# Optimization experiments

Measured on AMD Instinct MI355X. Metric: run time of the kernel, lower is better.

Reference implementation:

```python
import jax, jax.numpy as jnp
import numpy as np

B, L, H, E, V, X = 128, 1024, 256, 128, 50000, 100


def setup_inputs() -> dict:
    key = jax.random.key(0)
    ks = jax.random.split(key, 24)
    s = 0.02
    n = lambda k, shp: jax.random.normal(k, shp, dtype=jnp.float32) * s
    inp = {
        "y_t": jax.random.randint(ks[0], (B,), 0, V),
        "h0": n(ks[1], (B, H)),
        "c0": n(ks[2], (B, H)),
        "enc_outs": jax.random.normal(ks[3], (B, L, 2 * H), dtype=jnp.float32),
        "enc_feats": jax.random.normal(ks[4], (B * L, 2 * H), dtype=jnp.float32),
        "enc_padding_mask": jnp.ones((B, L), dtype=jnp.float32),
        "c_t_1": n(ks[5], (B, 2 * H)),
        "extra_zeros": jnp.zeros((B, X), dtype=jnp.float32),
        "enc_batch_extend_vocab": jax.random.randint(ks[6], (B, L), 0, V + X),
        "coverage": jnp.zeros((B, L), dtype=jnp.float32),
        # learned parameters (torch Linear convention: y = x @ W.T + b)
        "embed_W": n(ks[7], (V, E)),
        "Wih": n(ks[8], (4 * H, E)),
        "Whh": n(ks[9], (4 * H, H)),
        "bih": jnp.zeros((4 * H,), jnp.float32),
        "bhh": jnp.zeros((4 * H,), jnp.float32),
        "xctx_W": n(ks[10], (E, 2 * H + E)),
        "xctx_b": jnp.zeros((E,), jnp.float32),
        "Ws_W": n(ks[11], (2 * H, 2 * H)),
        "Ws_b": jnp.zeros((2 * H,), jnp.float32),
        "Wc_W": n(ks[12], (2 * H, 1)),
        "v_W": n(ks[13], (1, 2 * H)),
        "pgen_W": n(ks[14], (1, 4 * H + E)),
        "pgen_b": jnp.zeros((1,), jnp.float32),
        "proj_W": n(ks[15], (H, 3 * H)),
        "proj_b": jnp.zeros((H,), jnp.float32),
        "out_W": n(ks[16], (V, H)),
        "out_b": jnp.zeros((V,), jnp.float32),
    }
    return inp


def reference(y_t, h0, c0, enc_outs, enc_feats, enc_padding_mask, c_t_1,
              extra_zeros, enc_batch_extend_vocab, coverage,
              embed_W, Wih, Whh, bih, bhh, xctx_W, xctx_b, Ws_W, Ws_b,
              Wc_W, v_W, pgen_W, pgen_b, proj_W, proj_b, out_W, out_b):
    b, l = coverage.shape
    hd = h0.shape[1]
    # embedding + input-feeding context projection
    emb = embed_W[y_t]                                        # [B,E]
    x = jnp.concatenate([c_t_1, emb], axis=1) @ xctx_W.T + xctx_b  # [B,E]
    # single LSTM step (torch gate order i,f,g,o)
    gates = x @ Wih.T + bih + h0 @ Whh.T + bhh                # [B,4H]
    i_g, f_g, g_g, o_g = jnp.split(gates, 4, axis=1)
    c = jax.nn.sigmoid(f_g) * c0 + jax.nn.sigmoid(i_g) * jnp.tanh(g_g)
    h = jax.nn.sigmoid(o_g) * jnp.tanh(c)
    s_t_hat = jnp.concatenate([h, c], axis=1)                 # [B,2H]
    # coverage attention
    dec_feats = s_t_hat @ Ws_W.T + Ws_b                       # [B,2H]
    cov_feats = coverage.reshape(-1, 1) @ Wc_W.T              # [B*L,2H]
    feats = (enc_feats.reshape(b, l, 2 * hd)
             + dec_feats[:, None, :]
             + cov_feats.reshape(b, l, 2 * hd))
    energy = jnp.tanh(feats) @ v_W[0]                         # [B,L]
    a = jax.nn.softmax(energy, axis=1) * enc_padding_mask
    a = a / jnp.sum(a, axis=1, keepdims=True)
    c_t = jnp.einsum('bl,bld->bd', a, enc_outs)               # [B,2H]
    coverage_next = coverage + a
    # generation probability
    p_gen = jax.nn.sigmoid(
        jnp.concatenate([c_t, s_t_hat, x], axis=1) @ pgen_W.T + pgen_b)  # [B,1]
    # vocab distribution
    out_hid = jnp.concatenate([h, c_t], axis=1) @ proj_W.T + proj_b      # [B,H]
    logits = out_hid @ out_W.T + out_b                                    # [B,V]
    vocab_dist = p_gen * jax.nn.softmax(logits, axis=1)
    attn_dist_ = (1.0 - p_gen) * a
    # extended vocab + pointer scatter-add
    vd_ext = jnp.concatenate([vocab_dist, extra_zeros], axis=1)          # [B,V+X]
    rows = jnp.arange(b)[:, None]
    final_dist = vd_ext.at[rows, enc_batch_extend_vocab].add(attn_dist_)
    return (final_dist, h, c, c_t, a, p_gen, coverage_next)
```

## Files before the change

kernel.cpp:

```cpp
#include <hip/hip_runtime.h>
#include <hip/hip_bf16.h>
#include <cstdint>
#include <cstddef>

#define B_   128
#define L_   1024
#define H_   256
#define E_   128
#define V_   50000
#define X_   100
#define VX_  50100
#define LSTR 50112

#define OUT_H    6412800
#define OUT_C    6445568
#define OUT_CT   6478336
#define OUT_A    6543872
#define OUT_PGEN 6674944
#define OUT_COV  6675072

typedef __attribute__((ext_vector_type(8))) short bf16x8;
typedef __attribute__((ext_vector_type(4))) float f32x4;
typedef __attribute__((ext_vector_type(8))) unsigned short u16x8;

__device__ inline float bf2f(unsigned short u){
  union { unsigned int i; float f; } v; v.i = ((unsigned int)u) << 16; return v.f;
}
__device__ inline unsigned short f2bf(float f){
  union { float f; unsigned int i; } v; v.f = f;
  unsigned int lsb = (v.i >> 16) & 1u;
  v.i += 0x7fffu + lsb;
  return (unsigned short)(v.i >> 16);
}
__device__ inline float sigm(float x){ return __builtin_amdgcn_rcpf(1.f + __expf(-x)); }
__device__ inline float tanh_f(float x){
  float ax = fabsf(x);
  float t  = __expf(-2.f * ax);
  float r  = (1.f - t) * __builtin_amdgcn_rcpf(1.f + t);
  return copysignf(r, x);
}
__device__ inline float ldf(const void* p, size_t i, bool f32){
  return f32 ? ((const float*)p)[i] : bf2f(((const unsigned short*)p)[i]);
}
__device__ inline void stf(void* p, size_t i, float v, bool f32){
  if (f32) ((float*)p)[i] = v; else ((unsigned short*)p)[i] = f2bf(v);
}
__device__ inline void atomic_add_bf16(unsigned short* addr, float val){
  uintptr_t a = (uintptr_t)addr;
  unsigned int* word = (unsigned int*)(a & ~(uintptr_t)3);
  bool hi = (a & 2) != 0;
  unsigned int old = *word, assumed;
  do {
    assumed = old;
    unsigned short cur = hi ? (unsigned short)(assumed >> 16) : (unsigned short)(assumed & 0xffffu);
    unsigned short nv = f2bf(bf2f(cur) + val);
    unsigned int next = hi ? ((assumed & 0x0000ffffu) | ((unsigned int)nv << 16))
                           : ((assumed & 0xffff0000u) | (unsigned int)nv);
    old = atomicCAS(word, assumed, next);
  } while (old != assumed);
}

__global__ void k0_flag(const unsigned short* __restrict__ mask, int* __restrict__ flag){
  if (threadIdx.x == 0) flag[0] = (mask[0] == 0x3F80u) ? 0 : 1;
}

__global__ void k1_xctx(const int* __restrict__ y_t, const void* __restrict__ c_t_1,
                        const void* __restrict__ embed_W,
                        const void* __restrict__ xctx_W, const void* __restrict__ xctx_b,
                        const int* __restrict__ flag, float* __restrict__ x_ws){
  bool f32 = flag[0] != 0;
  int j = blockIdx.x;
  int m = threadIdx.x;
  size_t wr = (size_t)j * 640;
  size_t ct = (size_t)m * 512;
  size_t em = (size_t)y_t[m] * 128;
  float acc = ldf(xctx_b, j, f32);
  if (f32){
    const float* W = (const float*)xctx_W + wr;
    const float* C = (const float*)c_t_1 + ct;
    const float* Em = (const float*)embed_W + em;
    for (int k = 0; k < 512; ++k) acc += C[k] * W[k];
    for (int k = 0; k < 128; ++k) acc += Em[k] * W[512 + k];
  } else {
    const unsigned short* W = (const unsigned short*)xctx_W + wr;
    const unsigned short* C = (const unsigned short*)c_t_1 + ct;
    const unsigned short* Em = (const unsigned short*)embed_W + em;
    for (int k = 0; k < 512; ++k) acc += bf2f(C[k]) * bf2f(W[k]);
    for (int k = 0; k < 128; ++k) acc += bf2f(Em[k]) * bf2f(W[512 + k]);
  }
  x_ws[m * 128 + j] = acc;
}

__global__ void k2_lstm(const float* __restrict__ x_ws, const void* __restrict__ h0,
                        const void* __restrict__ c0,
                        const void* __restrict__ Wih, const void* __restrict__ Whh,
                        const void* __restrict__ bih, const void* __restrict__ bhh,
                        const int* __restrict__ flag, float* __restrict__ st_ws, void* __restrict__ out){
  bool f32 = flag[0] != 0;
  int j = blockIdx.x;
  int m = threadIdx.x;
  const float* xr = x_ws + m * 128;
  float g[4];
  if (f32){
    const float* hr = (const float*)h0 + m * 256;
    #pragma unroll
    for (int gi = 0; gi < 4; ++gi){
      int n = j + gi * 256;
      float acc = ((const float*)bih)[n] + ((const float*)bhh)[n];
      const float* wi = (const float*)Wih + (size_t)n * 128;
      const float* wh = (const float*)Whh + (size_t)n * 256;
      for (int k = 0; k < 128; ++k) acc += xr[k] * wi[k];
      for (int k = 0; k < 256; ++k) acc += hr[k] * wh[k];
      g[gi] = acc;
    }
  } else {
    const unsigned short* hr = (const unsigned short*)h0 + m * 256;
    #pragma unroll
    for (int gi = 0; gi < 4; ++gi){
      int n = j + gi * 256;
      float acc = bf2f(((const unsigned short*)bih)[n]) + bf2f(((const unsigned short*)bhh)[n]);
      const unsigned short* wi = (const unsigned short*)Wih + (size_t)n * 128;
      const unsigned short* wh = (const unsigned short*)Whh + (size_t)n * 256;
      for (int k = 0; k < 128; ++k) acc += xr[k] * bf2f(wi[k]);
      for (int k = 0; k < 256; ++k) acc += bf2f(hr[k]) * bf2f(wh[k]);
      g[gi] = acc;
    }
  }
  float c0v = ldf(c0, (size_t)m * 256 + j, f32);
  float c = sigm(g[1]) * c0v + sigm(g[0]) * tanh_f(g[2]);
  float h = sigm(g[3]) * tanh_f(c);
  st_ws[m * 512 + j]       = h;
  st_ws[m * 512 + 256 + j] = c;
  stf(out, (size_t)OUT_H + m * 256 + j, h, f32);
  stf(out, (size_t)OUT_C + m * 256 + j, c, f32);
}

__global__ void k3_decfeat(const float* __restrict__ st_ws, const void* __restrict__ Ws_W,
                           const void* __restrict__ Ws_b, const int* __restrict__ flag,
                           float* __restrict__ dec_ws){
  bool f32 = flag[0] != 0;
  int d = blockIdx.x;
  int m = threadIdx.x;
  const float* sr = st_ws + m * 512;
  float acc = ldf(Ws_b, d, f32);
  if (f32){
    const float* wr = (const float*)Ws_W + (size_t)d * 512;
    for (int k = 0; k < 512; ++k) acc += sr[k] * wr[k];
  } else {
    const unsigned short* wr = (const unsigned short*)Ws_W + (size_t)d * 512;
    for (int k = 0; k < 512; ++k) acc += sr[k] * bf2f(wr[k]);
  }
  dec_ws[m * 512 + d] = acc;
}

__global__ void k4_energy(const void* __restrict__ enc_feats, const float* __restrict__ dec_ws,
                          const void* __restrict__ coverage, const void* __restrict__ Wc,
                          const void* __restrict__ vW, const int* __restrict__ flag,
                          float* __restrict__ energy_ws){
  bool f32 = flag[0] != 0;
  int g = blockIdx.x * 4 + (threadIdx.x >> 6);
  int lane = threadIdx.x & 63;
  int b = g >> 10;
  int d0 = lane * 8;
  float vv[8], wc[8], ef[8];
  if (f32){
    const float* vp = (const float*)vW + d0;
    const float* wp = (const float*)Wc + d0;
    const float* ep = (const float*)enc_feats + (size_t)g * 512 + d0;
    float4 a0 = ((const float4*)vp)[0], a1 = ((const float4*)vp)[1];
    float4 b0 = ((const float4*)wp)[0], b1 = ((const float4*)wp)[1];
    float4 c0 = ((const float4*)ep)[0], c1 = ((const float4*)ep)[1];
    vv[0]=a0.x; vv[1]=a0.y; vv[2]=a0.z; vv[3]=a0.w; vv[4]=a1.x; vv[5]=a1.y; vv[6]=a1.z; vv[7]=a1.w;
    wc[0]=b0.x; wc[1]=b0.y; wc[2]=b0.z; wc[3]=b0.w; wc[4]=b1.x; wc[5]=b1.y; wc[6]=b1.z; wc[7]=b1.w;
    ef[0]=c0.x; ef[1]=c0.y; ef[2]=c0.z; ef[3]=c0.w; ef[4]=c1.x; ef[5]=c1.y; ef[6]=c1.z; ef[7]=c1.w;
  } else {
    u16x8 a = *(const u16x8*)((const unsigned short*)vW + d0);
    u16x8 w = *(const u16x8*)((const unsigned short*)Wc + d0);
    u16x8 e = *(const u16x8*)((const unsigned short*)enc_feats + (size_t)g * 512 + d0);
    #pragma unroll
    for (int jj = 0; jj < 8; ++jj){ vv[jj] = bf2f(a[jj]); wc[jj] = bf2f(w[jj]); ef[jj] = bf2f(e[jj]); }
  }
  const float4* dr = (const float4*)(dec_ws + b * 512 + d0);
  float4 dv0 = dr[0], dv1 = dr[1];
  float dec[8] = {dv0.x, dv0.y, dv0.z, dv0.w, dv1.x, dv1.y, dv1.z, dv1.w};
  float cov = ldf(coverage, g, f32);
  float acc = 0.f;
  #pragma unroll
  for (int jj = 0; jj < 8; ++jj){
    float f = ef[jj] + dec[jj] + cov * wc[jj];
    acc += tanh_f(f) * vv[jj];
  }
  #pragma unroll
  for (int off = 32; off > 0; off >>= 1) acc += __shfl_down(acc, off, 64);
  if (lane == 0) energy_ws[g] = acc;
}

__global__ void k5_attn(const float* __restrict__ energy_ws, const void* __restrict__ mask,
                        const void* __restrict__ coverage, const int* __restrict__ flag,
                        float* __restrict__ a_ws, float* __restrict__ ct_ws, void* __restrict__ out){
  bool f32 = flag[0] != 0;
  __shared__ float red[256];
  int b = blockIdx.x, t = threadIdx.x;
  const float* er = energy_ws + b * 1024;
  float e[4];
  float mx = -1e30f;
  #pragma unroll
  for (int i = 0; i < 4; ++i){ e[i] = er[t + i * 256]; mx = fmaxf(mx, e[i]); }
  red[t] = mx; __syncthreads();
  for (int s = 128; s > 0; s >>= 1){ if (t < s) red[t] = fmaxf(red[t], red[t + s]); __syncthreads(); }
  float M = red[0]; __syncthreads();
  float sum = 0.f;
  #pragma unroll
  for (int i = 0; i < 4; ++i){
    float mk = ldf(mask, (size_t)b * 1024 + t + i * 256, f32);
    e[i] = __expf(e[i] - M) * mk;
    sum += e[i];
  }
  red[t] = sum; __syncthreads();
  for (int s = 128; s > 0; s >>= 1){ if (t < s) red[t] += red[t + s]; __syncthreads(); }
  float inv = 1.f / red[0];
  #pragma unroll
  for (int i = 0; i < 4; ++i){
    int l = t + i * 256;
    float av = e[i] * inv;
    a_ws[b * 1024 + l] = av;
    stf(out, (size_t)OUT_A + b * 1024 + l, av, f32);
    stf(out, (size_t)OUT_COV + b * 1024 + l, ldf(coverage, (size_t)b * 1024 + l, f32) + av, f32);
  }
  ct_ws[b * 512 + t] = 0.f;
  ct_ws[b * 512 + t + 256] = 0.f;
}

__global__ void k6_ctx(const float* __restrict__ a_ws, const void* __restrict__ enc_outs,
                       const int* __restrict__ flag, float* __restrict__ ct_ws){
  bool f32 = flag[0] != 0;
  __shared__ float ash[256];
  int blk = blockIdx.x;
  int b = blk >> 2, part = blk & 3;
  int t = threadIdx.x;
  int l0 = part * 256;
  ash[t] = a_ws[b * 1024 + l0 + t];
  __syncthreads();
  int d = t * 2;
  float acc0 = 0.f, acc1 = 0.f;
  if (f32){
    const float* base = (const float*)enc_outs + ((size_t)(b * 1024 + l0)) * 512 + d;
    for (int l = 0; l < 256; ++l){
      float2 v = *(const float2*)(base + (size_t)l * 512);
      float a = ash[l];
      acc0 += a * v.x; acc1 += a * v.y;
    }
  } else {
    const unsigned short* base = (const unsigned short*)enc_outs + ((size_t)(b * 1024 + l0)) * 512 + d;
    for (int l = 0; l < 256; ++l){
      unsigned int pk = *(const unsigned int*)(base + (size_t)l * 512);
      float a = ash[l];
      acc0 += a * bf2f((unsigned short)(pk & 0xffffu));
      acc1 += a * bf2f((unsigned short)(pk >> 16));
    }
  }
  atomicAdd(&ct_ws[b * 512 + d],     acc0);
  atomicAdd(&ct_ws[b * 512 + d + 1], acc1);
}

__global__ void k7_pgen(const float* __restrict__ ct_ws, const float* __restrict__ st_ws,
                        const float* __restrict__ x_ws, const void* __restrict__ pgen_W,
                        const void* __restrict__ pgen_b, const int* __restrict__ flag,
                        float* __restrict__ pgen_ws, void* __restrict__ out){
  bool f32 = flag[0] != 0;
  __shared__ float red[256];
  int b = blockIdx.x, t = threadIdx.x;
  stf(out, (size_t)OUT_CT + b * 512 + t,       ct_ws[b * 512 + t], f32);
  stf(out, (size_t)OUT_CT + b * 512 + t + 256, ct_ws[b * 512 + t + 256], f32);
  float acc = 0.f;
  for (int k = t; k < 1152; k += 256){
    float v = (k < 512) ? ct_ws[b * 512 + k]
            : (k < 1024) ? st_ws[b * 512 + (k - 512)]
            : x_ws[b * 128 + (k - 1024)];
    acc += v * ldf(pgen_W, k, f32);
  }
  red[t] = acc; __syncthreads();
  for (int s = 128; s > 0; s >>= 1){ if (t < s) red[t] += red[t + s]; __syncthreads(); }
  if (t == 0){
    float p = sigm(red[0] + ldf(pgen_b, 0, f32));
    pgen_ws[b] = p;
    stf(out, (size_t)OUT_PGEN + b, p, f32);
  }
}

__global__ void k8_outhid(const float* __restrict__ st_ws, const float* __restrict__ ct_ws,
                          const void* __restrict__ proj_W, const void* __restrict__ proj_b,
                          const int* __restrict__ flag, unsigned short* __restrict__ outhid_bf){
  bool f32 = flag[0] != 0;
  int i = blockIdx.x;
  int m = threadIdx.x;
  float acc = ldf(proj_b, i, f32);
  const float* hr = st_ws + m * 512;
  const float* cr = ct_ws + m * 512;
  if (f32){
    const float* wr = (const float*)proj_W + (size_t)i * 768;
    for (int k = 0; k < 256; ++k) acc += hr[k] * wr[k];
    for (int k = 0; k < 512; ++k) acc += cr[k] * wr[256 + k];
  } else {
    const unsigned short* wr = (const unsigned short*)proj_W + (size_t)i * 768;
    for (int k = 0; k < 256; ++k) acc += hr[k] * bf2f(wr[k]);
    for (int k = 0; k < 512; ++k) acc += cr[k] * bf2f(wr[256 + k]);
  }
  outhid_bf[m * 256 + i] = f2bf(acc);
}

__global__ void k9_logits(const unsigned short* __restrict__ outhid_bf, const void* __restrict__ out_W,
                          const void* __restrict__ out_b, const int* __restrict__ flag,
                          unsigned short* __restrict__ logits_bf){
  bool f32 = flag[0] != 0;
  int wid = blockIdx.x * 4 + (threadIdx.x >> 6);
  if (wid >= V_ / 16) return;
  int lane = threadIdx.x & 63;
  int q = lane >> 4, r = lane & 15;
  int n0 = wid * 16;
  const bf16x8* Ar = (const bf16x8*)(outhid_bf);
  float bias = ldf(out_b, n0 + r, f32);
  f32x4 acc[8];
  #pragma unroll
  for (int mt = 0; mt < 8; ++mt) acc[mt] = (f32x4){0.f, 0.f, 0.f, 0.f};
  #pragma unroll
  for (int kk = 0; kk < 8; ++kk){
    bf16x8 bfrag;
    if (f32){
      const float* wf = (const float*)out_W + (size_t)(n0 + r) * 256 + kk * 32 + q * 8;
      float4 w0 = ((const float4*)wf)[0], w1 = ((const float4*)wf)[1];
      bfrag[0] = (short)f2bf(w0.x); bfrag[1] = (short)f2bf(w0.y);
      bfrag[2] = (short)f2bf(w0.z); bfrag[3] = (short)f2bf(w0.w);
      bfrag[4] = (short)f2bf(w1.x); bfrag[5] = (short)f2bf(w1.y);
      bfrag[6] = (short)f2bf(w1.z); bfrag[7] = (short)f2bf(w1.w);
    } else {
      bfrag = ((const bf16x8*)((const unsigned short*)out_W + (size_t)(n0 + r) * 256))[kk * 4 + q];
    }
    #pragma unroll
    for (int mt = 0; mt < 8; ++mt){
      bf16x8 afrag = Ar[(mt * 16 + r) * 32 + kk * 4 + q];
      acc[mt] = __builtin_amdgcn_mfma_f32_16x16x32_bf16(afrag, bfrag, acc[mt], 0, 0, 0);
    }
  }
  #pragma unroll
  for (int mt = 0; mt < 8; ++mt){
    #pragma unroll
    for (int rr = 0; rr < 4; ++rr){
      int m = mt * 16 + q * 4 + rr;
      logits_bf[(size_t)m * LSTR + n0 + r] = f2bf(acc[mt][rr] + bias);
    }
  }
}

__global__ void k10_rowred(const unsigned short* __restrict__ logits_bf, float* __restrict__ pm, float* __restrict__ ps){
  __shared__ float red[256];
  int blk = blockIdx.x;
  int b = blk >> 2, part = blk & 3;
  int t = threadIdx.x;
  const unsigned short* row = logits_bf + (size_t)b * LSTR + part * 12500;
  float mx = -1e30f;
  for (int c = t; c < 12500; c += 256) mx = fmaxf(mx, bf2f(row[c]));
  red[t] = mx; __syncthreads();
  for (int s = 128; s > 0; s >>= 1){ if (t < s) red[t] = fmaxf(red[t], red[t + s]); __syncthreads(); }
  float M = red[0]; __syncthreads();
  float sum = 0.f;
  for (int c = t; c < 12500; c += 256) sum += __expf(bf2f(row[c]) - M);
  red[t] = sum; __syncthreads();
  for (int s = 128; s > 0; s >>= 1){ if (t < s) red[t] += red[t + s]; __syncthreads(); }
  if (t == 0){ pm[blk] = M; ps[blk] = red[0]; }
}

__global__ void k10b_merge(const float* __restrict__ pm, const float* __restrict__ ps,
                           const float* __restrict__ pgen_ws, float* __restrict__ rm, float* __restrict__ rs){
  int b = threadIdx.x;
  float M = fmaxf(fmaxf(pm[b * 4], pm[b * 4 + 1]), fmaxf(pm[b * 4 + 2], pm[b * 4 + 3]));
  float S = 0.f;
  for (int p = 0; p < 4; ++p) S += ps[b * 4 + p] * __expf(pm[b * 4 + p] - M);
  rm[b] = M;
  rs[b] = pgen_ws[b] / S;
}

__global__ void k11_vocab(const unsigned short* __restrict__ logits_bf, const float* __restrict__ rm,
                          const float* __restrict__ rs, const int* __restrict__ flag, void* __restrict__ out){
  bool f32 = flag[0] != 0;
  int b = blockIdx.y, t = threadIdx.x;
  int c0 = blockIdx.x * 2048 + t * 8;
  if (c0 >= VX_) return;
  const unsigned short* lrow = logits_bf + (size_t)b * LSTR;
  float M = rm[b], S = rs[b];
  #pragma unroll
  for (int j = 0; j < 8; ++j){
    int c = c0 + j;
    if (c < VX_){
      float v = (c < V_) ? __expf(bf2f(lrow[c]) - M) * S : 0.f;
      stf(out, (size_t)b * VX_ + c, v, f32);
    }
  }
}

__global__ void k12_scatter(const int* __restrict__ ebev, const float* __restrict__ a_ws,
                            const float* __restrict__ pgen_ws, const int* __restrict__ flag,
                            void* __restrict__ out){
  bool f32 = flag[0] != 0;
  int g = blockIdx.x * 256 + threadIdx.x;
  int b = g >> 10;
  float val = (1.f - pgen_ws[b]) * a_ws[g];
  size_t idx = (size_t)b * VX_ + ebev[g];
  if (f32) atomicAdd((float*)out + idx, val);
  else     atomic_add_bf16((unsigned short*)out + idx, val);
}

extern "C" void kernel_launch(void* const* d_in, const int* in_sizes, int n_in,
                              void* d_out, int out_size, void* d_ws, size_t ws_size,
                              hipStream_t stream){
  const int*  y_t   = (const int*)d_in[0];
  const void* h0    = d_in[1];
  const void* c0    = d_in[2];
  const void* enc_outs  = d_in[3];
  const void* enc_feats = d_in[4];
  const void* mask  = d_in[5];
  const void* c_t_1 = d_in[6];
  const int*  ebev  = (const int*)d_in[8];
  const void* coverage = d_in[9];
  const void* embed_W = d_in[10];
  const void* Wih   = d_in[11];
  const void* Whh   = d_in[12];
  const void* bih   = d_in[13];
  const void* bhh   = d_in[14];
  const void* xctx_W = d_in[15];
  const void* xctx_b = d_in[16];
  const void* Ws_W  = d_in[17];
  const void* Ws_b  = d_in[18];
  const void* Wc_W  = d_in[19];
  const void* v_W   = d_in[20];
  const void* pgen_W = d_in[21];
  const void* pgen_b = d_in[22];
  const void* proj_W = d_in[23];
  const void* proj_b = d_in[24];
  const void* out_W = d_in[25];
  const void* out_b = d_in[26];

  float* ws        = (float*)d_ws;
  float* x_ws      = ws;
  float* st_ws     = ws + 16384;
  float* dec_ws    = ws + 81920;
  float* energy_ws = ws + 147456;
  float* a_ws      = ws + 278528;
  float* ct_ws     = ws + 409600;
  float* pgen_ws   = ws + 475136;
  float* pm_ws     = ws + 475264;
  float* ps_ws     = ws + 475776;
  float* rm_ws     = ws + 476288;
  float* rs_ws     = ws + 476416;
  int*   flag_ws   = (int*)(ws + 476544);
  unsigned short* outhid_bf = (unsigned short*)(ws + 476576);
  unsigned short* logits_bf = (unsigned short*)(ws + 492960);

  k0_flag  <<<1, 64, 0, stream>>>((const unsigned short*)mask, flag_ws);
  k1_xctx  <<<128, 128, 0, stream>>>(y_t, c_t_1, embed_W, xctx_W, xctx_b, flag_ws, x_ws);
  k2_lstm  <<<256, 128, 0, stream>>>(x_ws, h0, c0, Wih, Whh, bih, bhh, flag_ws, st_ws, d_out);
  k3_decfeat<<<512, 128, 0, stream>>>(st_ws, Ws_W, Ws_b, flag_ws, dec_ws);
  k4_energy<<<32768, 256, 0, stream>>>(enc_feats, dec_ws, coverage, Wc_W, v_W, flag_ws, energy_ws);
  k5_attn  <<<128, 256, 0, stream>>>(energy_ws, mask, coverage, flag_ws, a_ws, ct_ws, d_out);
  k6_ctx   <<<512, 256, 0, stream>>>(a_ws, enc_outs, flag_ws, ct_ws);
  k7_pgen  <<<128, 256, 0, stream>>>(ct_ws, st_ws, x_ws, pgen_W, pgen_b, flag_ws, pgen_ws, d_out);
  k8_outhid<<<256, 128, 0, stream>>>(st_ws, ct_ws, proj_W, proj_b, flag_ws, outhid_bf);
  k9_logits<<<(V_ / 16 + 3) / 4, 256, 0, stream>>>(outhid_bf, out_W, out_b, flag_ws, logits_bf);
  k10_rowred<<<512, 256, 0, stream>>>(logits_bf, pm_ws, ps_ws);
  k10b_merge<<<1, 128, 0, stream>>>(pm_ws, ps_ws, pgen_ws, rm_ws, rs_ws);
  k11_vocab<<<dim3(25, 128), 256, 0, stream>>>(logits_bf, rm_ws, rs_ws, flag_ws, d_out);
  k12_scatter<<<512, 256, 0, stream>>>(ebev, a_ws, pgen_ws, flag_ws, d_out);
}
```

Measured before the change: 795.1 us.

## Pre-transpose small weight matrices and restructure dense GEMVs for coalesced access

Adds a pre-pass kernel that transposes xctx, LSTM gate, Ws and proj weights into fp32 K-major workspace buffers and sums the two LSTM biases. The small dense kernels now use one block per batch row, stage the activations in shared memory and read the transposed weights coalesced across threads, replacing per-thread strided row walks. The dtype flag kernel and the softmax merge kernel are removed: each kernel checks the mask directly and k11 merges the partial softmax stats inline. The transpose runs on every call and costs extra memory traffic and one extra launch.

```diff
diff --git a/kernel.cpp b/kernel.cpp
--- a/kernel.cpp
+++ b/kernel.cpp
@@ -38,6 +38,9 @@
   float t  = __expf(-2.f * ax);
   float r  = (1.f - t) * __builtin_amdgcn_rcpf(1.f + t);
   return copysignf(r, x);
+}
+__device__ inline bool is_f32m(const void* mask){
+  return ((const unsigned short*)mask)[0] != 0x3F80u;
 }
 __device__ inline float ldf(const void* p, size_t i, bool f32){
   return f32 ? ((const float*)p)[i] : bf2f(((const unsigned short*)p)[i]);
@@ -60,104 +63,108 @@
   } while (old != assumed);
 }
 
-__global__ void k0_flag(const unsigned short* __restrict__ mask, int* __restrict__ flag){
-  if (threadIdx.x == 0) flag[0] = (mask[0] == 0x3F80u) ? 0 : 1;
+__global__ void k_pre(const void* __restrict__ xctx_W, const void* __restrict__ Wih,
+                      const void* __restrict__ Whh, const void* __restrict__ Ws_W,
+                      const void* __restrict__ proj_W, const void* __restrict__ bih,
+                      const void* __restrict__ bhh, const void* __restrict__ mask,
+                      float* __restrict__ xctxT, float* __restrict__ gatesT,
+                      float* __restrict__ bg, float* __restrict__ WsT,
+                      float* __restrict__ projT){
+  bool f32 = is_f32m(mask);
+  const int total = 81920 + 131072 + 262144 + 262144 + 196608 + 1024;
+  for (int e = blockIdx.x * 256 + threadIdx.x; e < total; e += gridDim.x * 256){
+    int r = e;
+    if (r < 81920){
+      int n = r / 640, k = r - n * 640;
+      xctxT[k * 128 + n] = ldf(xctx_W, r, f32);
+    } else if ((r -= 81920) < 131072){
+      int n = r >> 7, k = r & 127;
+      gatesT[k * 1024 + n] = ldf(Wih, r, f32);
+    } else if ((r -= 131072) < 262144){
+      int n = r >> 8, k = r & 255;
+      gatesT[(128 + k) * 1024 + n] = ldf(Whh, r, f32);
+    } else if ((r -= 262144) < 262144){
+      int n = r >> 9, k = r & 511;
+      WsT[k * 512 + n] = ldf(Ws_W, r, f32);
+    } else if ((r -= 262144) < 196608){
+      int n = r / 768, k = r - n * 768;
+      projT[k * 256 + n] = ldf(proj_W, r, f32);
+    } else {
+      r -= 196608;
+      bg[r] = ldf(bih, r, f32) + ldf(bhh, r, f32);
+    }
+  }
 }
 
 __global__ void k1_xctx(const int* __restrict__ y_t, const void* __restrict__ c_t_1,
-                        const void* __restrict__ embed_W,
-                        const void* __restrict__ xctx_W, const void* __restrict__ xctx_b,
-                        const int* __restrict__ flag, float* __restrict__ x_ws){
-  bool f32 = flag[0] != 0;
-  int j = blockIdx.x;
-  int m = threadIdx.x;
-  size_t wr = (size_t)j * 640;
-  size_t ct = (size_t)m * 512;
+                        const void* __restrict__ embed_W, const float* __restrict__ xctxT,
+                        const void* __restrict__ xctx_b, const void* __restrict__ mask,
+                        float* __restrict__ x_ws){
+  bool f32 = is_f32m(mask);
+  __shared__ float act[640];
+  int m = blockIdx.x, t = threadIdx.x;
+  for (int k = t; k < 512; k += 128) act[k] = ldf(c_t_1, (size_t)m * 512 + k, f32);
   size_t em = (size_t)y_t[m] * 128;
-  float acc = ldf(xctx_b, j, f32);
-  if (f32){
-    const float* W = (const float*)xctx_W + wr;
-    const float* C = (const float*)c_t_1 + ct;
-    const float* Em = (const float*)embed_W + em;
-    for (int k = 0; k < 512; ++k) acc += C[k] * W[k];
-    for (int k = 0; k < 128; ++k) acc += Em[k] * W[512 + k];
-  } else {
-    const unsigned short* W = (const unsigned short*)xctx_W + wr;
-    const unsigned short* C = (const unsigned short*)c_t_1 + ct;
-    const unsigned short* Em = (const unsigned short*)embed_W + em;
-    for (int k = 0; k < 512; ++k) acc += bf2f(C[k]) * bf2f(W[k]);
-    for (int k = 0; k < 128; ++k) acc += bf2f(Em[k]) * bf2f(W[512 + k]);
-  }
-  x_ws[m * 128 + j] = acc;
+  act[512 + t] = ldf(embed_W, em + t, f32);
+  __syncthreads();
+  float acc = ldf(xctx_b, t, f32);
+  for (int k = 0; k < 640; ++k) acc += act[k] * xctxT[k * 128 + t];
+  x_ws[m * 128 + t] = acc;
 }
 
 __global__ void k2_lstm(const float* __restrict__ x_ws, const void* __restrict__ h0,
-                        const void* __restrict__ c0,
-                        const void* __restrict__ Wih, const void* __restrict__ Whh,
-                        const void* __restrict__ bih, const void* __restrict__ bhh,
-                        const int* __restrict__ flag, float* __restrict__ st_ws, void* __restrict__ out){
-  bool f32 = flag[0] != 0;
-  int j = blockIdx.x;
-  int m = threadIdx.x;
-  const float* xr = x_ws + m * 128;
+                        const void* __restrict__ c0, const float* __restrict__ gatesT,
+                        const float* __restrict__ bg, const void* __restrict__ mask,
+                        float* __restrict__ st_ws, void* __restrict__ out){
+  bool f32 = is_f32m(mask);
+  __shared__ float act[384];
+  int m = blockIdx.x, t = threadIdx.x;
+  if (t < 128) act[t] = x_ws[m * 128 + t];
+  act[128 + t] = ldf(h0, (size_t)m * 256 + t, f32);
+  __syncthreads();
   float g[4];
-  if (f32){
-    const float* hr = (const float*)h0 + m * 256;
+  #pragma unroll
+  for (int gi = 0; gi < 4; ++gi) g[gi] = bg[t + gi * 256];
+  for (int k = 0; k < 384; ++k){
+    float a = act[k];
+    const float* wr = gatesT + (size_t)k * 1024 + t;
     #pragma unroll
-    for (int gi = 0; gi < 4; ++gi){
-      int n = j + gi * 256;
-      float acc = ((const float*)bih)[n] + ((const float*)bhh)[n];
-      const float* wi = (const float*)Wih + (size_t)n * 128;
-      const float* wh = (const float*)Whh + (size_t)n * 256;
-      for (int k = 0; k < 128; ++k) acc += xr[k] * wi[k];
-      for (int k = 0; k < 256; ++k) acc += hr[k] * wh[k];
-      g[gi] = acc;
-    }
-  } else {
-    const unsigned short* hr = (const unsigned short*)h0 + m * 256;
-    #pragma unroll
-    for (int gi = 0; gi < 4; ++gi){
-      int n = j + gi * 256;
-      float acc = bf2f(((const unsigned short*)bih)[n]) + bf2f(((const unsigned short*)bhh)[n]);
-      const unsigned short* wi = (const unsigned short*)Wih + (size_t)n * 128;
-      const unsigned short* wh = (const unsigned short*)Whh + (size_t)n * 256;
-      for (int k = 0; k < 128; ++k) acc += xr[k] * bf2f(wi[k]);
-      for (int k = 0; k < 256; ++k) acc += bf2f(hr[k]) * bf2f(wh[k]);
-      g[gi] = acc;
-    }
-  }
-  float c0v = ldf(c0, (size_t)m * 256 + j, f32);
+    for (int gi = 0; gi < 4; ++gi) g[gi] += a * wr[gi * 256];
+  }
+  float c0v = ldf(c0, (size_t)m * 256 + t, f32);
   float c = sigm(g[1]) * c0v + sigm(g[0]) * tanh_f(g[2]);
   float h = sigm(g[3]) * tanh_f(c);
-  st_ws[m * 512 + j]       = h;
-  st_ws[m * 512 + 256 + j] = c;
-  stf(out, (size_t)OUT_H + m * 256 + j, h, f32);
-  stf(out, (size_t)OUT_C + m * 256 + j, c, f32);
-}
-
-__global__ void k3_decfeat(const float* __restrict__ st_ws, const void* __restrict__ Ws_W,
-                           const void* __restrict__ Ws_b, const int* __restrict__ flag,
+  st_ws[m * 512 + t]       = h;
+  st_ws[m * 512 + 256 + t] = c;
+  stf(out, (size_t)OUT_H + m * 256 + t, h, f32);
+  stf(out, (size_t)OUT_C + m * 256 + t, c, f32);
+}
+
+__global__ void k3_decfeat(const float* __restrict__ st_ws, const float* __restrict__ WsT,
+                           const void* __restrict__ Ws_b, const void* __restrict__ mask,
                            float* __restrict__ dec_ws){
-  bool f32 = flag[0] != 0;
-  int d = blockIdx.x;
-  int m = threadIdx.x;
-  const float* sr = st_ws + m * 512;
-  float acc = ldf(Ws_b, d, f32);
-  if (f32){
-    const float* wr = (const float*)Ws_W + (size_t)d * 512;
-    for (int k = 0; k < 512; ++k) acc += sr[k] * wr[k];
-  } else {
-    const unsigned short* wr = (const unsigned short*)Ws_W + (size_t)d * 512;
-    for (int k = 0; k < 512; ++k) acc += sr[k] * bf2f(wr[k]);
-  }
-  dec_ws[m * 512 + d] = acc;
+  bool f32 = is_f32m(mask);
+  __shared__ float act[512];
+  int m = blockIdx.x, t = threadIdx.x;
+  act[t]       = st_ws[m * 512 + t];
+  act[256 + t] = st_ws[m * 512 + 256 + t];
+  __syncthreads();
+  float a0 = ldf(Ws_b, t, f32), a1 = ldf(Ws_b, t + 256, f32);
+  for (int k = 0; k < 512; ++k){
+    float a = act[k];
+    const float* wr = WsT + (size_t)k * 512 + t;
+    a0 += a * wr[0];
+    a1 += a * wr[256];
+  }
+  dec_ws[m * 512 + t]       = a0;
+  dec_ws[m * 512 + 256 + t] = a1;
 }
 
 __global__ void k4_energy(const void* __restrict__ enc_feats, const float* __restrict__ dec_ws,
                           const void* __restrict__ coverage, const void* __restrict__ Wc,
-                          const void* __restrict__ vW, const int* __restrict__ flag,
+                          const void* __restrict__ vW, const void* __restrict__ mask,
                           float* __restrict__ energy_ws){
-  bool f32 = flag[0] != 0;
+  bool f32 = is_f32m(mask);
   int g = blockIdx.x * 4 + (threadIdx.x >> 6);
   int lane = threadIdx.x & 63;
   int b = g >> 10;
@@ -196,9 +203,9 @@
 }
 
 __global__ void k5_attn(const float* __restrict__ energy_ws, const void* __restrict__ mask,
-                        const void* __restrict__ coverage, const int* __restrict__ flag,
+                        const void* __restrict__ coverage,
                         float* __restrict__ a_ws, float* __restrict__ ct_ws, void* __restrict__ out){
-  bool f32 = flag[0] != 0;
+  bool f32 = is_f32m(mask);
   __shared__ float red[256];
   int b = blockIdx.x, t = threadIdx.x;
   const float* er = energy_ws + b * 1024;
@@ -232,8 +239,8 @@
 }
 
 __global__ void k6_ctx(const float* __restrict__ a_ws, const void* __restrict__ enc_outs,
-                       const int* __restrict__ flag, float* __restrict__ ct_ws){
-  bool f32 = flag[0] != 0;
+                       const void* __restrict__ mask, float* __restrict__ ct_ws){
+  bool f32 = is_f32m(mask);
   __shared__ float ash[256];
   int blk = blockIdx.x;
   int b = blk >> 2, part = blk & 3;
@@ -265,9 +272,9 @@
 
 __global__ void k7_pgen(const float* __restrict__ ct_ws, const float* __restrict__ st_ws,
                         const float* __restrict__ x_ws, const void* __restrict__ pgen_W,
-                        const void* __restrict__ pgen_b, const int* __restrict__ flag,
+                        const void* __restrict__ pgen_b, const void* __restrict__ mask,
                         float* __restrict__ pgen_ws, void* __restrict__ out){
-  bool f32 = flag[0] != 0;
+  bool f32 = is_f32m(mask);
   __shared__ float red[256];
   int b = blockIdx.x, t = threadIdx.x;
   stf(out, (size_t)OUT_CT + b * 512 + t,       ct_ws[b * 512 + t], f32);
@@ -289,30 +296,24 @@
 }
 
 __global__ void k8_outhid(const float* __restrict__ st_ws, const float* __restrict__ ct_ws,
-                          const void* __restrict__ proj_W, const void* __restrict__ proj_b,
-                          const int* __restrict__ flag, unsigned short* __restrict__ outhid_bf){
-  bool f32 = flag[0] != 0;
-  int i = blockIdx.x;
-  int m = threadIdx.x;
-  float acc = ldf(proj_b, i, f32);
-  const float* hr = st_ws + m * 512;
-  const float* cr = ct_ws + m * 512;
-  if (f32){
-    const float* wr = (const float*)proj_W + (size_t)i * 768;
-    for (int k = 0; k < 256; ++k) acc += hr[k] * wr[k];
-    for (int k = 0; k < 512; ++k) acc += cr[k] * wr[256 + k];
-  } else {
-    const unsigned short* wr = (const unsigned short*)proj_W + (size_t)i * 768;
-    for (int k = 0; k < 256; ++k) acc += hr[k] * bf2f(wr[k]);
-    for (int k = 0; k < 512; ++k) acc += cr[k] * bf2f(wr[256 + k]);
-  }
-  outhid_bf[m * 256 + i] = f2bf(acc);
+                          const float* __restrict__ projT, const void* __restrict__ proj_b,
+                          const void* __restrict__ mask, unsigned short* __restrict__ outhid_bf){
+  bool f32 = is_f32m(mask);
+  __shared__ float act[768];
+  int m = blockIdx.x, t = threadIdx.x;
+  act[t]       = st_ws[m * 512 + t];
+  act[256 + t] = ct_ws[m * 512 + t];
+  act[512 + t] = ct_ws[m * 512 + 256 + t];
+  __syncthreads();
+  float acc = ldf(proj_b, t, f32);
+  for (int k = 0; k < 768; ++k) acc += act[k] * projT[k * 256 + t];
+  outhid_bf[m * 256 + t] = f2bf(acc);
 }
 
 __global__ void k9_logits(const unsigned short* __restrict__ outhid_bf, const void* __restrict__ out_W,
-                          const void* __restrict__ out_b, const int* __restrict__ flag,
+                          const void* __restrict__ out_b, const void* __restrict__ mask,
                           unsigned short* __restrict__ logits_bf){
-  bool f32 = flag[0] != 0;
+  bool f32 = is_f32m(mask);
   int wid = blockIdx.x * 4 + (threadIdx.x >> 6);
   if (wid >= V_ / 16) return;
   int lane = threadIdx.x & 63;
@@ -370,38 +371,33 @@
   if (t == 0){ pm[blk] = M; ps[blk] = red[0]; }
 }
 
-__global__ void k10b_merge(const float* __restrict__ pm, const float* __restrict__ ps,
-                           const float* __restrict__ pgen_ws, float* __restrict__ rm, float* __restrict__ rs){
-  int b = threadIdx.x;
+__global__ void k11_vocab(const unsigned short* __restrict__ logits_bf, const float* __restrict__ pm,
+                          const float* __restrict__ ps, const float* __restrict__ pgen_ws,
+                          const void* __restrict__ mask, void* __restrict__ out){
+  bool f32 = is_f32m(mask);
+  int b = blockIdx.y, t = threadIdx.x;
   float M = fmaxf(fmaxf(pm[b * 4], pm[b * 4 + 1]), fmaxf(pm[b * 4 + 2], pm[b * 4 + 3]));
   float S = 0.f;
+  #pragma unroll
   for (int p = 0; p < 4; ++p) S += ps[b * 4 + p] * __expf(pm[b * 4 + p] - M);
-  rm[b] = M;
-  rs[b] = pgen_ws[b] / S;
-}
-
-__global__ void k11_vocab(const unsigned short* __restrict__ logits_bf, const float* __restrict__ rm,
-                          const float* __restrict__ rs, const int* __restrict__ flag, void* __restrict__ out){
-  bool f32 = flag[0] != 0;
-  int b = blockIdx.y, t = threadIdx.x;
+  float Sc = pgen_ws[b] / S;
   int c0 = blockIdx.x * 2048 + t * 8;
   if (c0 >= VX_) return;
   const unsigned short* lrow = logits_bf + (size_t)b * LSTR;
-  float M = rm[b], S = rs[b];
   #pragma unroll
   for (int j = 0; j < 8; ++j){
     int c = c0 + j;
     if (c < VX_){
-      float v = (c < V_) ? __expf(bf2f(lrow[c]) - M) * S : 0.f;
+      float v = (c < V_) ? __expf(bf2f(lrow[c]) - M) * Sc : 0.f;
       stf(out, (size_t)b * VX_ + c, v, f32);
     }
   }
 }
 
 __global__ void k12_scatter(const int* __restrict__ ebev, const float* __restrict__ a_ws,
-                            const float* __restrict__ pgen_ws, const int* __restrict__ flag,
+                            const float* __restrict__ pgen_ws, const void* __restrict__ mask,
                             void* __restrict__ out){
-  bool f32 = flag[0] != 0;
+  bool f32 = is_f32m(mask);
   int g = blockIdx.x * 256 + threadIdx.x;
   int b = g >> 10;
   float val = (1.f - pgen_ws[b]) * a_ws[g];
@@ -450,24 +446,26 @@
   float* pgen_ws   = ws + 475136;
   float* pm_ws     = ws + 475264;
   float* ps_ws     = ws + 475776;
-  float* rm_ws     = ws + 476288;
-  float* rs_ws     = ws + 476416;
-  int*   flag_ws   = (int*)(ws + 476544);
   unsigned short* outhid_bf = (unsigned short*)(ws + 476576);
   unsigned short* logits_bf = (unsigned short*)(ws + 492960);
-
-  k0_flag  <<<1, 64, 0, stream>>>((const unsigned short*)mask, flag_ws);
-  k1_xctx  <<<128, 128, 0, stream>>>(y_t, c_t_1, embed_W, xctx_W, xctx_b, flag_ws, x_ws);
-  k2_lstm  <<<256, 128, 0, stream>>>(x_ws, h0, c0, Wih, Whh, bih, bhh, flag_ws, st_ws, d_out);
-  k3_decfeat<<<512, 128, 0, stream>>>(st_ws, Ws_W, Ws_b, flag_ws, dec_ws);
-  k4_energy<<<32768, 256, 0, stream>>>(enc_feats, dec_ws, coverage, Wc_W, v_W, flag_ws, energy_ws);
-  k5_attn  <<<128, 256, 0, stream>>>(energy_ws, mask, coverage, flag_ws, a_ws, ct_ws, d_out);
-  k6_ctx   <<<512, 256, 0, stream>>>(a_ws, enc_outs, flag_ws, ct_ws);
-  k7_pgen  <<<128, 256, 0, stream>>>(ct_ws, st_ws, x_ws, pgen_W, pgen_b, flag_ws, pgen_ws, d_out);
-  k8_outhid<<<256, 128, 0, stream>>>(st_ws, ct_ws, proj_W, proj_b, flag_ws, outhid_bf);
-  k9_logits<<<(V_ / 16 + 3) / 4, 256, 0, stream>>>(outhid_bf, out_W, out_b, flag_ws, logits_bf);
+  float* xctxT     = ws + 3700128;
+  float* gatesT    = ws + 3782048;
+  float* bg_ws     = ws + 4175264;
+  float* WsT       = ws + 4176288;
+  float* projT     = ws + 4438432;
+
+  k_pre    <<<1024, 256, 0, stream>>>(xctx_W, Wih, Whh, Ws_W, proj_W, bih, bhh, mask,
+                                      xctxT, gatesT, bg_ws, WsT, projT);
+  k1_xctx  <<<128, 128, 0, stream>>>(y_t, c_t_1, embed_W, xctxT, xctx_b, mask, x_ws);
+  k2_lstm  <<<128, 256, 0, stream>>>(x_ws, h0, c0, gatesT, bg_ws, mask, st_ws, d_out);
+  k3_decfeat<<<128, 256, 0, stream>>>(st_ws, WsT, Ws_b, mask, dec_ws);
+  k4_energy<<<32768, 256, 0, stream>>>(enc_feats, dec_ws, coverage, Wc_W, v_W, mask, energy_ws);
+  k5_attn  <<<128, 256, 0, stream>>>(energy_ws, mask, coverage, a_ws, ct_ws, d_out);
+  k6_ctx   <<<512, 256, 0, stream>>>(a_ws, enc_outs, mask, ct_ws);
+  k7_pgen  <<<128, 256, 0, stream>>>(ct_ws, st_ws, x_ws, pgen_W, pgen_b, mask, pgen_ws, d_out);
+  k8_outhid<<<128, 256, 0, stream>>>(st_ws, ct_ws, projT, proj_b, mask, outhid_bf);
+  k9_logits<<<(V_ / 16 + 3) / 4, 256, 0, stream>>>(outhid_bf, out_W, out_b, mask, logits_bf);
   k10_rowred<<<512, 256, 0, stream>>>(logits_bf, pm_ws, ps_ws);
-  k10b_merge<<<1, 128, 0, stream>>>(pm_ws, ps_ws, pgen_ws, rm_ws, rs_ws);
-  k11_vocab<<<dim3(25, 128), 256, 0, stream>>>(logits_bf, rm_ws, rs_ws, flag_ws, d_out);
-  k12_scatter<<<512, 256, 0, stream>>>(ebev, a_ws, pgen_ws, flag_ws, d_out);
-}
+  k11_vocab<<<dim3(25, 128), 256, 0, stream>>>(logits_bf, pm_ws, ps_ws, pgen_ws, mask, d_out);
+  k12_scatter<<<512, 256, 0, stream>>>(ebev, a_ws, pgen_ws, mask, d_out);
+}
```

Result: faster. 775.7 us (-2.4%).
